# Optimization experiments

Measured on AMD Instinct MI355X. Metric: run time of the kernel, lower is better.

## Reference

```python
import jax, jax.numpy as jnp
import numpy as np

NHEAD = 8
NEG_INF = -1e9
LN_EPS = 1e-5


def setup_inputs() -> dict:
    key = jax.random.key(0)
    ks = jax.random.split(key, 8)
    B, Q, N, C = 2, 256, 16384, 256
    return {
        "queries": jax.random.normal(ks[0], (B, Q, C), jnp.float32),
        "vid_features": jax.random.normal(ks[1], (B, C, N), jnp.float32),
        "vid_mask": jax.random.uniform(ks[2], (B, Q, N), jnp.float32),
        "pos_embed": jax.random.normal(ks[3], (B, C, N), jnp.float32),
        "query_embed": jax.random.normal(ks[4], (B, Q, C), jnp.float32),
        "in_proj_w": jax.random.normal(ks[5], (3 * C, C), jnp.float32) * 0.02,
        "in_proj_b": jnp.zeros((3 * C,), jnp.float32),
        "out_proj_w": jax.random.normal(ks[6], (C, C), jnp.float32) * 0.02,
        "out_proj_b": jnp.zeros((C,), jnp.float32),
        "ln_gamma": jnp.ones((C,), jnp.float32),
        "ln_beta": jnp.zeros((C,), jnp.float32),
    }


def reference(queries, vid_features, vid_mask, pos_embed, query_embed,
              in_proj_w, in_proj_b, out_proj_w, out_proj_b, ln_gamma, ln_beta):
    B, Q, C = queries.shape
    H = NHEAD
    d = C // H

    vf = jnp.transpose(vid_features, (0, 2, 1))   # B N C
    pe = jnp.transpose(pos_embed, (0, 2, 1))      # B N C

    q_in = queries + query_embed                  # with_pos_embed on queries
    k_in = vf + pe                                # with_pos_embed on keys
    v_in = vf

    wq, wk, wv = jnp.split(in_proj_w, 3, axis=0)
    bq, bk, bv = jnp.split(in_proj_b, 3)

    q = (q_in @ wq.T + bq).reshape(B, Q, H, d)
    k = (k_in @ wk.T + bk).reshape(B, -1, H, d)
    v = (v_in @ wv.T + bv).reshape(B, -1, H, d)

    scale = 1.0 / jnp.sqrt(jnp.asarray(d, q.dtype))
    logits = jnp.einsum('bqhd,bnhd->bhqn', q, k) * scale  # B H Q N

    # Hard masking: block keys where mask prob < 0.5; if a query row is
    # fully blocked, fall back to unmasked attention (avoid NaN softmax).
    blocked = vid_mask < 0.5                                 # B Q N
    all_blocked = jnp.all(blocked, axis=-1, keepdims=True)   # B Q 1
    blocked = blocked & jnp.logical_not(all_blocked)
    logits = jnp.where(blocked[:, None, :, :], NEG_INF, logits)

    attn = jax.nn.softmax(logits, axis=-1)
    ctx = jnp.einsum('bhqn,bnhd->bqhd', attn, v).reshape(B, Q, C)
    tgt2 = ctx @ out_proj_w.T + out_proj_b

    # residual + LayerNorm (dropout p=0.0 -> identity)
    x = queries + tgt2
    mu = jnp.mean(x, axis=-1, keepdims=True)
    var = jnp.mean(jnp.square(x - mu), axis=-1, keepdims=True)
    return (x - mu) / jnp.sqrt(var + LN_EPS) * ln_gamma + ln_beta
```

## Files before the change

kernel.cpp:

```cpp
#include <hip/hip_runtime.h>
#include <stdint.h>

#define B_ 2
#define Q_ 256
#define N_ 16384
#define C_ 256
#define H_ 8
#define D_ 32
#define NC_ 32
#define SCALE 0.17677669529663687f

typedef __bf16 bf16x8 __attribute__((ext_vector_type(8)));
typedef float f32x4 __attribute__((ext_vector_type(4)));

__device__ __forceinline__ uint16_t bfbits(float f) {
  union { __bf16 h; uint16_t u; } c;
  c.h = (__bf16)f;
  return c.u;
}
__device__ __forceinline__ uint16_t f2bf(float f) {
  union { float f; uint32_t u; } c; c.f = f;
  uint32_t r = c.u + 0x7FFFu + ((c.u >> 16) & 1u);
  return (uint16_t)(r >> 16);
}
__device__ __forceinline__ uint32_t pk2(float a, float b) {
  return (uint32_t)f2bf(a) | ((uint32_t)f2bf(b) << 16);
}
__device__ __forceinline__ void lgkm0_barrier() {
  __builtin_amdgcn_sched_barrier(0);
  asm volatile("s_waitcnt lgkmcnt(0)" ::: "memory");
  __builtin_amdgcn_sched_barrier(0);
  __builtin_amdgcn_s_barrier();
  __builtin_amdgcn_sched_barrier(0);
}

__global__ __launch_bounds__(256) void prep(const float* __restrict__ inw,
                                            const float* __restrict__ outw,
                                            const float* __restrict__ vm,
                                            uint16_t* __restrict__ wb,
                                            float* __restrict__ woT,
                                            uint32_t* __restrict__ mb) {
  __shared__ __align__(16) char sh[4352];
  const int bid = blockIdx.x;
  const int t = threadIdx.x;
  if (bid < 96) {
    const int i = (bid * 256 + t) * 8;
    const float4 a = *reinterpret_cast<const float4*>(inw + i);
    const float4 b = *reinterpret_cast<const float4*>(inw + i + 4);
    ushort4 lo = {bfbits(a.x), bfbits(a.y), bfbits(a.z), bfbits(a.w)};
    ushort4 hi = {bfbits(b.x), bfbits(b.y), bfbits(b.z), bfbits(b.w)};
    *reinterpret_cast<ushort4*>(wb + i) = lo;
    *reinterpret_cast<ushort4*>(wb + i + 4) = hi;
  } else if (bid < 160) {
    float(*s)[33] = reinterpret_cast<float(*)[33]>(sh);
    const int bb = bid - 96;
    const int bx = bb & 7, by = bb >> 3;
    const int r0 = by * 32, c0 = bx * 32;
    const int tr = t >> 5, tc = t & 31;
#pragma unroll
    for (int k = 0; k < 4; ++k)
      s[tr + 8 * k][tc] = outw[(size_t)(r0 + tr + 8 * k) * 256 + c0 + tc];
    __syncthreads();
#pragma unroll
    for (int k = 0; k < 4; ++k)
      woT[(size_t)(c0 + tr + 8 * k) * 256 + r0 + tc] = s[tc][tr + 8 * k];
  } else {
    uint8_t(*nib)[256] = reinterpret_cast<uint8_t(*)[256]>(sh);
    __shared__ int wcnt[4];
    __shared__ int tot;
    const int bq = bid - 160;
    const float* row = vm + (size_t)bq * N_;
    const int lane = t & 63;
    int cnt = 0;
#pragma unroll
    for (int i = 0; i < 16; ++i) {
      const float4 v = *reinterpret_cast<const float4*>(&row[i * 1024 + 4 * t]);
      const uint32_t nb = (v.x < 0.5f ? 1u : 0u) | (v.y < 0.5f ? 2u : 0u) |
                          (v.z < 0.5f ? 4u : 0u) | (v.w < 0.5f ? 8u : 0u);
      nib[i][t] = (uint8_t)nb;
      cnt += __popc(nb);
    }
    for (int o = 32; o > 0; o >>= 1) cnt += __shfl_down(cnt, o, 64);
    if (lane == 0) wcnt[t >> 6] = cnt;
    __syncthreads();
    if (t == 0) tot = wcnt[0] + wcnt[1] + wcnt[2] + wcnt[3];
    __syncthreads();
    const bool allb = (tot == N_);
    uint32_t* dst = mb + (size_t)bq * 512;
#pragma unroll
    for (int k = 0; k < 2; ++k) {
      const int w = k * 256 + t;
      const int i = w >> 5, tw = w & 31;
      const uint2 u = *reinterpret_cast<const uint2*>(&nib[i][8 * tw]);
      uint32_t y0 = u.x & 0x0F0F0F0Fu; y0 = y0 | (y0 >> 4);
      uint32_t y1 = u.y & 0x0F0F0F0Fu; y1 = y1 | (y1 >> 4);
      const uint32_t word = (y0 & 0xFFu) | (((y0 >> 16) & 0xFFu) << 8) |
                            ((y1 & 0xFFu) << 16) | (((y1 >> 16) & 0xFFu) << 24);
      dst[w] = allb ? 0u : word;
    }
  }
}

__global__ __launch_bounds__(512) void kvqproj(const float* __restrict__ vf,
                                               const float* __restrict__ pe,
                                               const float* __restrict__ queries,
                                               const float* __restrict__ qembed,
                                               const uint16_t* __restrict__ wkv,
                                               const float* __restrict__ bias,
                                               uint16_t* __restrict__ Kb,
                                               uint16_t* __restrict__ Vb,
                                               uint16_t* __restrict__ Qb) {
  __shared__ __align__(16) uint16_t lds[8][64][40];
  const int bid = blockIdx.x;
  const int t = threadIdx.x, wid = t >> 6, lane = t & 63;
  const int g = lane >> 4, c15 = lane & 15;

  if (bid < 1024) {
    const int nb = bid & 511, b = bid >> 9;
    const int n0 = nb * 32;
    const int cin = t >> 1, nh = (t & 1) * 16;
    const int s = cin >> 5, cl = cin & 31;
    const float* Xrow = vf + ((size_t)b * C_ + cin) * N_ + n0 + nh;
    const float* Prow = pe + ((size_t)b * C_ + cin) * N_ + n0 + nh;
    float4 xr4[4], pr4[4];
#pragma unroll
    for (int k = 0; k < 4; ++k) xr4[k] = reinterpret_cast<const float4*>(Xrow)[k];
#pragma unroll
    for (int k = 0; k < 4; ++k) pr4[k] = reinterpret_cast<const float4*>(Prow)[k];
    const float* xf = reinterpret_cast<const float*>(xr4);
    const float* pf = reinterpret_cast<const float*>(pr4);
#pragma unroll
    for (int i = 0; i < 16; ++i) {
      const int n = nh + i;
      const int col = cl ^ (8 * ((n >> 3) & 3));
      lds[s][n][col] = bfbits(xf[i] + pf[i]);
      lds[s][32 + n][col] = bfbits(xf[i]);
    }
    lgkm0_barrier();

    const bool isK = wid < 4;
    const int wc = wid & 3;
    const uint16_t* W = wkv + (isK ? 256 * C_ : 512 * C_);
    f32x4 acc[4][2];
    if (isK) {
#pragma unroll
      for (int cf = 0; cf < 4; ++cf) {
        f32x4 iv;
#pragma unroll
        for (int j = 0; j < 4; ++j) iv[j] = bias[256 + wc * 64 + cf * 16 + 4 * g + j];
        acc[cf][0] = iv;
        acc[cf][1] = iv;
      }
    } else {
#pragma unroll
      for (int cf = 0; cf < 4; ++cf) {
        const float bv = bias[512 + wc * 64 + cf * 16 + c15];
        const f32x4 iv = {bv, bv, bv, bv};
        acc[0][cf] = iv;
        acc[1][cf] = iv;
      }
    }
#pragma unroll
    for (int s8 = 0; s8 < 8; ++s8) {
      bf16x8 Wf[4];
#pragma unroll
      for (int cf = 0; cf < 4; ++cf)
        Wf[cf] = *reinterpret_cast<const bf16x8*>(
            W + (size_t)(wc * 64 + cf * 16 + c15) * C_ + s8 * 32 + g * 8);
      if (isK) {
#pragma unroll
        for (int nf = 0; nf < 2; ++nf) {
          const int r = nf * 16 + c15;
          const bf16x8 Bf = *reinterpret_cast<const bf16x8*>(
              &lds[s8][r][8 * (g ^ ((r >> 3) & 3))]);
#pragma unroll
          for (int cf = 0; cf < 4; ++cf)
            acc[cf][nf] = __builtin_amdgcn_mfma_f32_16x16x32_bf16(Wf[cf], Bf, acc[cf][nf], 0, 0, 0);
        }
      } else {
#pragma unroll
        for (int nf = 0; nf < 2; ++nf) {
          const int r = nf * 16 + c15;
          const bf16x8 Af = *reinterpret_cast<const bf16x8*>(
              &lds[s8][32 + r][8 * (g ^ ((r >> 3) & 3))]);
#pragma unroll
          for (int cf = 0; cf < 4; ++cf)
            acc[nf][cf] = __builtin_amdgcn_mfma_f32_16x16x32_bf16(Af, Wf[cf], acc[nf][cf], 0, 0, 0);
        }
      }
    }
    if (isK) {
      uint16_t* Kp = Kb + (size_t)b * N_ * C_;
#pragma unroll
      for (int cf = 0; cf < 4; ++cf)
#pragma unroll
        for (int nf = 0; nf < 2; ++nf) {
          const f32x4 a = acc[cf][nf];
          uint2 pkv;
          pkv.x = pk2(a[0], a[1]);
          pkv.y = pk2(a[2], a[3]);
          *reinterpret_cast<uint2*>(
              &Kp[(size_t)(n0 + nf * 16 + c15) * C_ + wc * 64 + cf * 16 + 4 * g]) = pkv;
        }
    } else {
      uint16_t* Vp = Vb + (size_t)b * C_ * N_;
#pragma unroll
      for (int nf = 0; nf < 2; ++nf)
#pragma unroll
        for (int cf = 0; cf < 4; ++cf) {
          const f32x4 a = acc[nf][cf];
          uint2 pkv;
          pkv.x = pk2(a[0], a[1]);
          pkv.y = pk2(a[2], a[3]);
          *reinterpret_cast<uint2*>(
              &Vp[(size_t)(wc * 64 + cf * 16 + c15) * N_ + n0 + nf * 16 + 4 * g]) = pkv;
        }
    }
  } else {
    const int qb = bid - 1024;
    const int q0g = qb * 64;
    const int b = q0g >> 8, q0 = q0g & 255;
    const int r = t >> 3, c0 = (t & 7) * 32, s = t & 7;
    const float* Qrow = queries + (size_t)(q0g + r) * C_ + c0;
    const float* Erow = qembed + (size_t)(q0g + r) * C_ + c0;
#pragma unroll
    for (int ph = 0; ph < 2; ++ph) {
      float4 a4[4], e4[4];
#pragma unroll
      for (int k = 0; k < 4; ++k) a4[k] = reinterpret_cast<const float4*>(Qrow + ph * 16)[k];
#pragma unroll
      for (int k = 0; k < 4; ++k) e4[k] = reinterpret_cast<const float4*>(Erow + ph * 16)[k];
      const float* af = reinterpret_cast<const float*>(a4);
      const float* ef = reinterpret_cast<const float*>(e4);
#pragma unroll
      for (int i = 0; i < 16; ++i) {
        const int cl = ph * 16 + i;
        const int col = cl ^ (8 * ((r >> 3) & 3));
        lds[s][r][col] = bfbits(af[i] + ef[i]);
      }
      __builtin_amdgcn_sched_barrier(0);
    }
    lgkm0_barrier();

    const int w = wid;
    f32x4 acc[4][2];
#pragma unroll
    for (int nf = 0; nf < 2; ++nf) {
      const float bv = bias[w * 32 + nf * 16 + c15];
      const f32x4 iv = {bv, bv, bv, bv};
#pragma unroll
      for (int qf = 0; qf < 4; ++qf) acc[qf][nf] = iv;
    }
#pragma unroll
    for (int s8 = 0; s8 < 8; ++s8) {
      bf16x8 Bf[2];
#pragma unroll
      for (int nf = 0; nf < 2; ++nf)
        Bf[nf] = *reinterpret_cast<const bf16x8*>(
            wkv + (size_t)(w * 32 + nf * 16 + c15) * C_ + s8 * 32 + g * 8);
#pragma unroll
      for (int qf = 0; qf < 4; ++qf) {
        const int rr = qf * 16 + c15;
        const bf16x8 Af = *reinterpret_cast<const bf16x8*>(
            &lds[s8][rr][8 * (g ^ ((rr >> 3) & 3))]);
#pragma unroll
        for (int nf = 0; nf < 2; ++nf)
          acc[qf][nf] = __builtin_amdgcn_mfma_f32_16x16x32_bf16(Af, Bf[nf], acc[qf][nf], 0, 0, 0);
      }
    }
#pragma unroll
    for (int qf = 0; qf < 4; ++qf)
#pragma unroll
      for (int nf = 0; nf < 2; ++nf)
#pragma unroll
        for (int j = 0; j < 4; ++j) {
          const int q = q0 + qf * 16 + 4 * g + j;
          const int dk = nf * 16 + c15;
          Qb[((size_t)(b * H_ + w) * Q_ + q) * D_ + dk] = f2bf(acc[qf][nf][j] * SCALE);
        }
  }
}

__global__ __launch_bounds__(512) void attn(const uint16_t* __restrict__ Qb,
                                            const uint16_t* __restrict__ Kb,
                                            const uint16_t* __restrict__ Vb,
                                            const uint32_t* __restrict__ mb,
                                            float* __restrict__ ctx_part,
                                            float* __restrict__ lsum_part) {
  const int bid = blockIdx.x;
  const int nc = bid & 31, h = (bid >> 5) & 7, b = bid >> 8;
  const int t = threadIdx.x, wid = t >> 6, lane = t & 63;
  const int g = lane >> 4, c15 = lane & 15;
  const int qw0 = wid * 32;
  const int nbase = nc * (N_ / NC_);
  constexpr int SS = (N_ / NC_) / 128;

  __shared__ __align__(16) uint16_t kst[2][128][40];
  __shared__ __align__(16) uint16_t vst[2][32][136];
  __shared__ __align__(16) uint16_t plds[8][32][40];

  const uint16_t* Qp = Qb + (size_t)(b * H_ + h) * Q_ * D_;
  bf16x8 qfr[2];
#pragma unroll
  for (int qf = 0; qf < 2; ++qf)
    qfr[qf] = *reinterpret_cast<const bf16x8*>(Qp + (size_t)(qw0 + qf * 16 + c15) * D_ + g * 8);

  f32x4 acc[2][2];
  const f32x4 zero4 = {0.f, 0.f, 0.f, 0.f};
#pragma unroll
  for (int qf = 0; qf < 2; ++qf)
#pragma unroll
    for (int dvf = 0; dvf < 2; ++dvf) acc[qf][dvf] = zero4;
  float lsum[2][4] = {};

  const uint32_t* mrow = mb + (size_t)b * Q_ * (N_ / 32);

  const int krow = t >> 2, kch = t & 3;
  const uint16_t* ksrc = Kb + ((size_t)(b * N_ + nbase + krow)) * C_ + h * D_ + kch * 8;
  const int vrow = t >> 4, vch = t & 15;
  const uint16_t* vsrc = Vb + ((size_t)(b * C_ + h * D_ + vrow)) * N_ + nbase + vch * 8;

  uint4 kreg = *(const uint4*)ksrc;
  uint4 vreg = *(const uint4*)vsrc;

  int cur = 0;
  for (int ss = 0; ss < SS; ++ss) {
    *(uint4*)&kst[cur][krow][kch * 8] = kreg;
    *(uint4*)&vst[cur][vrow][vch * 8] = vreg;
    if (ss < SS - 1) {
      kreg = *(const uint4*)(ksrc + (size_t)(ss + 1) * 128 * C_);
      vreg = *(const uint4*)(vsrc + (ss + 1) * 128);
    }
    lgkm0_barrier();

    const int nstart = nbase + ss * 128;
#pragma unroll
    for (int half = 0; half < 2; ++half) {
      uint32_t mw[2][4][2];
#pragma unroll
      for (int qf = 0; qf < 2; ++qf)
#pragma unroll
        for (int j = 0; j < 4; ++j) {
          const int q = qw0 + qf * 16 + 4 * g + j;
          const uint2 u = *reinterpret_cast<const uint2*>(
              &mrow[(size_t)q * (N_ / 32) + (nstart >> 5) + half * 2]);
          mw[qf][j][0] = u.x;
          mw[qf][j][1] = u.y;
        }
#pragma unroll
      for (int s2 = 0; s2 < 2; ++s2) {
        const int sub = half * 2 + s2;
        const int nl0 = sub * 32;
        bf16x8 kfr[2];
#pragma unroll
        for (int nf = 0; nf < 2; ++nf)
          kfr[nf] = *reinterpret_cast<const bf16x8*>(&kst[cur][nl0 + nf * 16 + c15][g * 8]);
        f32x4 s[2][2];
#pragma unroll
        for (int qf = 0; qf < 2; ++qf)
#pragma unroll
          for (int nf = 0; nf < 2; ++nf)
            s[qf][nf] = __builtin_amdgcn_mfma_f32_16x16x32_bf16(qfr[qf], kfr[nf], zero4, 0, 0, 0);

#pragma unroll
        for (int qf = 0; qf < 2; ++qf) {
#pragma unroll
          for (int j = 0; j < 4; ++j) {
            const uint32_t wmask = mw[qf][j][s2];
#pragma unroll
            for (int nf = 0; nf < 2; ++nf) {
              const int bit = nf * 16 + c15;
              const float p = ((wmask >> bit) & 1u) ? 0.0f : __expf(s[qf][nf][j]);
              lsum[qf][j] += p;
              plds[wid][qf * 16 + 4 * g + j][nf * 16 + c15] = f2bf(p);
            }
          }
        }
        __asm__ volatile("s_waitcnt lgkmcnt(0)" ::: "memory");
#pragma unroll
        for (int qf = 0; qf < 2; ++qf) {
          const bf16x8 pa = *reinterpret_cast<const bf16x8*>(&plds[wid][qf * 16 + c15][g * 8]);
#pragma unroll
          for (int dvf = 0; dvf < 2; ++dvf) {
            const bf16x8 vb =
                *reinterpret_cast<const bf16x8*>(&vst[cur][dvf * 16 + c15][nl0 + g * 8]);
            acc[qf][dvf] = __builtin_amdgcn_mfma_f32_16x16x32_bf16(pa, vb, acc[qf][dvf], 0, 0, 0);
          }
        }
      }
    }
    __builtin_amdgcn_sched_barrier(0);
    cur ^= 1;
  }

#pragma unroll
  for (int qf = 0; qf < 2; ++qf)
#pragma unroll
    for (int j = 0; j < 4; ++j) {
      float v = lsum[qf][j];
      v += __shfl_xor(v, 1, 64);
      v += __shfl_xor(v, 2, 64);
      v += __shfl_xor(v, 4, 64);
      v += __shfl_xor(v, 8, 64);
      lsum[qf][j] = v;
    }

  float* cp = ctx_part + ((size_t)(b * H_ + h) * NC_ + nc) * Q_ * D_;
#pragma unroll
  for (int qf = 0; qf < 2; ++qf)
#pragma unroll
    for (int dvf = 0; dvf < 2; ++dvf)
#pragma unroll
      for (int j = 0; j < 4; ++j) {
        const int q = qw0 + qf * 16 + 4 * g + j;
        cp[(size_t)q * D_ + dvf * 16 + c15] = acc[qf][dvf][j];
      }
  if (c15 == 0) {
    float* lp = lsum_part + ((size_t)(b * H_ + h) * NC_ + nc) * Q_;
#pragma unroll
    for (int qf = 0; qf < 2; ++qf)
#pragma unroll
      for (int j = 0; j < 4; ++j) lp[qw0 + qf * 16 + 4 * g + j] = lsum[qf][j];
  }
}

__global__ __launch_bounds__(256) void epilogue(const float* __restrict__ ctx_part,
                                                const float* __restrict__ lsum_part,
                                                const float* __restrict__ queries,
                                                const float* __restrict__ woT,
                                                const float* __restrict__ bo,
                                                const float* __restrict__ gamma,
                                                const float* __restrict__ beta,
                                                float* __restrict__ out) {
  const int bq = blockIdx.x;
  const int b = bq >> 8, q = bq & 255;
  const int t = threadIdx.x;
  const int h = t >> 5, dv = t & 31;
  float cs = 0.f, ls = 0.f;
  for (int k = 0; k < NC_; ++k) {
    cs += ctx_part[(((size_t)(b * H_ + h) * NC_ + k) * Q_ + q) * D_ + dv];
    ls += lsum_part[((size_t)(b * H_ + h) * NC_ + k) * Q_ + q];
  }
  __shared__ float ctxrow[C_];
  ctxrow[t] = cs / ls;
  __syncthreads();
  float acc = bo[t];
#pragma unroll 8
  for (int j = 0; j < C_; ++j) acc = fmaf(ctxrow[j], woT[(size_t)j * C_ + t], acc);
  const float x = queries[(size_t)bq * C_ + t] + acc;
  float s1 = x, s2 = x * x;
  for (int o = 32; o > 0; o >>= 1) {
    s1 += __shfl_down(s1, o, 64);
    s2 += __shfl_down(s2, o, 64);
  }
  __shared__ float r1[4], r2[4];
  if ((t & 63) == 0) { r1[t >> 6] = s1; r2[t >> 6] = s2; }
  __syncthreads();
  const float mu = (r1[0] + r1[1] + r1[2] + r1[3]) * (1.0f / C_);
  const float e2 = (r2[0] + r2[1] + r2[2] + r2[3]) * (1.0f / C_);
  const float var = e2 - mu * mu;
  out[(size_t)bq * C_ + t] = (x - mu) * rsqrtf(var + 1e-5f) * gamma[t] + beta[t];
}

extern "C" void kernel_launch(void* const* d_in, const int* in_sizes, int n_in,
                              void* d_out, int out_size, void* d_ws, size_t ws_size,
                              hipStream_t stream) {
  const float* queries    = (const float*)d_in[0];
  const float* vidfeat    = (const float*)d_in[1];
  const float* vidmask    = (const float*)d_in[2];
  const float* posembed   = (const float*)d_in[3];
  const float* queryembed = (const float*)d_in[4];
  const float* inw        = (const float*)d_in[5];
  const float* inb        = (const float*)d_in[6];
  const float* outw       = (const float*)d_in[7];
  const float* outb       = (const float*)d_in[8];
  const float* gamma      = (const float*)d_in[9];
  const float* beta       = (const float*)d_in[10];
  float* out = (float*)d_out;

  char* ws = (char*)d_ws;
  size_t off = 0;
  uint16_t* Qb = (uint16_t*)(ws + off); off += (size_t)B_ * H_ * Q_ * D_ * 2;
  uint16_t* Kb = (uint16_t*)(ws + off); off += (size_t)B_ * N_ * C_ * 2;
  uint16_t* Vb = (uint16_t*)(ws + off); off += (size_t)B_ * C_ * N_ * 2;
  uint32_t* mb = (uint32_t*)(ws + off); off += (size_t)B_ * Q_ * (N_ / 32) * 4;
  float* ctxp  = (float*)(ws + off);    off += (size_t)B_ * H_ * NC_ * Q_ * D_ * 4;
  float* lsump = (float*)(ws + off);    off += (size_t)B_ * H_ * NC_ * Q_ * 4;
  uint16_t* wkv = (uint16_t*)(ws + off); off += (size_t)768 * C_ * 2;
  float* woT   = (float*)(ws + off);    off += (size_t)C_ * C_ * 4;

  prep<<<dim3(672), dim3(256), 0, stream>>>(inw, outw, vidmask, wkv, woT, mb);
  kvqproj<<<dim3(1032), dim3(512), 0, stream>>>(vidfeat, posembed, queries, queryembed,
                                                wkv, inb, Kb, Vb, Qb);
  attn<<<dim3(B_ * H_ * NC_), dim3(512), 0, stream>>>(Qb, Kb, Vb, mb, ctxp, lsump);
  epilogue<<<dim3(B_ * Q_), dim3(256), 0, stream>>>(ctxp, lsump, queries, woT, outb, gamma, beta, out);
}
```

Measured before the change: 111.5 us.

## Split K/V projection into bf16 pre-pack pass and register-pipelined GEMMs

The fused K/V/Q projection kernel is split up. A new pass adds the position embedding, converts activations to bf16 and writes them in a channel-group-interleaved layout. Two templated GEMM kernels then read that layout straight into registers, with software-pipelined weight loads, and write K and V in per-head contiguous layouts that the attention kernel now reads. Q projection moves to a scalar fp32 path using a transposed Wq, and the attention partial-sum buffers alias the staging buffers. The aim is to drop the LDS staging and transpose from the projection, at the cost of an extra round trip through global memory and two more launches.

```diff
diff --git a/kernel.cpp b/kernel.cpp
--- a/kernel.cpp
+++ b/kernel.cpp
@@ -39,6 +39,7 @@
                                             const float* __restrict__ vm,
                                             uint16_t* __restrict__ wb,
                                             float* __restrict__ woT,
+                                            float* __restrict__ wqT,
                                             uint32_t* __restrict__ mb) {
   __shared__ __align__(16) char sh[4352];
   const int bid = blockIdx.x;
@@ -47,28 +48,31 @@
     const int i = (bid * 256 + t) * 8;
     const float4 a = *reinterpret_cast<const float4*>(inw + i);
     const float4 b = *reinterpret_cast<const float4*>(inw + i + 4);
-    ushort4 lo = {bfbits(a.x), bfbits(a.y), bfbits(a.z), bfbits(a.w)};
-    ushort4 hi = {bfbits(b.x), bfbits(b.y), bfbits(b.z), bfbits(b.w)};
+    ushort4 lo = {f2bf(a.x), f2bf(a.y), f2bf(a.z), f2bf(a.w)};
+    ushort4 hi = {f2bf(b.x), f2bf(b.y), f2bf(b.z), f2bf(b.w)};
     *reinterpret_cast<ushort4*>(wb + i) = lo;
     *reinterpret_cast<ushort4*>(wb + i + 4) = hi;
-  } else if (bid < 160) {
+  } else if (bid < 224) {
     float(*s)[33] = reinterpret_cast<float(*)[33]>(sh);
-    const int bb = bid - 96;
+    const bool isWo = bid < 160;
+    const int bb = bid - (isWo ? 96 : 160);
+    const float* src = isWo ? outw : inw;
+    float* dst = isWo ? woT : wqT;
     const int bx = bb & 7, by = bb >> 3;
     const int r0 = by * 32, c0 = bx * 32;
     const int tr = t >> 5, tc = t & 31;
 #pragma unroll
     for (int k = 0; k < 4; ++k)
-      s[tr + 8 * k][tc] = outw[(size_t)(r0 + tr + 8 * k) * 256 + c0 + tc];
+      s[tr + 8 * k][tc] = src[(size_t)(r0 + tr + 8 * k) * 256 + c0 + tc];
     __syncthreads();
 #pragma unroll
     for (int k = 0; k < 4; ++k)
-      woT[(size_t)(c0 + tr + 8 * k) * 256 + r0 + tc] = s[tc][tr + 8 * k];
+      dst[(size_t)(c0 + tr + 8 * k) * 256 + r0 + tc] = s[tc][tr + 8 * k];
   } else {
     uint8_t(*nib)[256] = reinterpret_cast<uint8_t(*)[256]>(sh);
     __shared__ int wcnt[4];
     __shared__ int tot;
-    const int bq = bid - 160;
+    const int bq = bid - 224;
     const float* row = vm + (size_t)bq * N_;
     const int lane = t & 63;
     int cnt = 0;
@@ -101,189 +105,192 @@
   }
 }
 
-__global__ __launch_bounds__(512) void kvqproj(const float* __restrict__ vf,
-                                               const float* __restrict__ pe,
-                                               const float* __restrict__ queries,
-                                               const float* __restrict__ qembed,
-                                               const uint16_t* __restrict__ wkv,
-                                               const float* __restrict__ bias,
-                                               uint16_t* __restrict__ Kb,
-                                               uint16_t* __restrict__ Vb,
-                                               uint16_t* __restrict__ Qb) {
-  __shared__ __align__(16) uint16_t lds[8][64][40];
+__global__ __launch_bounds__(256) void fuse(const float* __restrict__ vf,
+                                            const float* __restrict__ pe,
+                                            const float* __restrict__ queries,
+                                            const float* __restrict__ qembed,
+                                            const float* __restrict__ wqT,
+                                            const float* __restrict__ bias,
+                                            uint16_t* __restrict__ XP,
+                                            uint16_t* __restrict__ XV,
+                                            uint16_t* __restrict__ Qb) {
   const int bid = blockIdx.x;
+  const int t = threadIdx.x;
+  if (bid < 1024) {
+    const int b = bid >> 9, cg = (bid >> 4) & 31, ch = bid & 15;
+    const int nq = ch * 1024 + t * 4;
+    const float* vb = vf + ((size_t)(b * 32 + cg) * 8) * N_ + nq;
+    const float* pb = pe + ((size_t)(b * 32 + cg) * 8) * N_ + nq;
+    float4 x[8], p[8];
+#pragma unroll
+    for (int r = 0; r < 8; ++r) x[r] = *reinterpret_cast<const float4*>(vb + (size_t)r * N_);
+#pragma unroll
+    for (int r = 0; r < 8; ++r) p[r] = *reinterpret_cast<const float4*>(pb + (size_t)r * N_);
+    uint16_t* xpo = XP + ((size_t)(b * 32 + cg) * N_ + nq) * 8;
+    uint16_t* xvo = XV + ((size_t)(b * 32 + cg) * N_ + nq) * 8;
+#pragma unroll
+    for (int i = 0; i < 4; ++i) {
+      const float* fx[8];
+      uint4 up, uv;
+      const float x0 = ((const float*)&x[0])[i], x1 = ((const float*)&x[1])[i];
+      const float x2 = ((const float*)&x[2])[i], x3 = ((const float*)&x[3])[i];
+      const float x4 = ((const float*)&x[4])[i], x5 = ((const float*)&x[5])[i];
+      const float x6 = ((const float*)&x[6])[i], x7 = ((const float*)&x[7])[i];
+      const float p0 = ((const float*)&p[0])[i], p1 = ((const float*)&p[1])[i];
+      const float p2 = ((const float*)&p[2])[i], p3 = ((const float*)&p[3])[i];
+      const float p4 = ((const float*)&p[4])[i], p5 = ((const float*)&p[5])[i];
+      const float p6 = ((const float*)&p[6])[i], p7 = ((const float*)&p[7])[i];
+      up.x = pk2(x0 + p0, x1 + p1); up.y = pk2(x2 + p2, x3 + p3);
+      up.z = pk2(x4 + p4, x5 + p5); up.w = pk2(x6 + p6, x7 + p7);
+      uv.x = pk2(x0, x1); uv.y = pk2(x2, x3);
+      uv.z = pk2(x4, x5); uv.w = pk2(x6, x7);
+      *reinterpret_cast<uint4*>(xpo + (size_t)i * 8) = up;
+      *reinterpret_cast<uint4*>(xvo + (size_t)i * 8) = uv;
+      (void)fx;
+    }
+  } else {
+    const int r0 = (bid - 1024) * 4;
+    __shared__ float xq[4][C_];
+#pragma unroll
+    for (int r = 0; r < 4; ++r)
+      xq[r][t] = queries[(size_t)(r0 + r) * C_ + t] + qembed[(size_t)(r0 + r) * C_ + t];
+    __syncthreads();
+    float a0 = bias[t], a1 = a0, a2 = a0, a3 = a0;
+#pragma unroll 4
+    for (int j = 0; j < C_; ++j) {
+      const float wv = wqT[(size_t)j * C_ + t];
+      a0 = fmaf(xq[0][j], wv, a0);
+      a1 = fmaf(xq[1][j], wv, a1);
+      a2 = fmaf(xq[2][j], wv, a2);
+      a3 = fmaf(xq[3][j], wv, a3);
+    }
+    const int h = t >> 5, dk = t & 31;
+    const float r4[4] = {a0, a1, a2, a3};
+#pragma unroll
+    for (int r = 0; r < 4; ++r) {
+      const int bq = r0 + r;
+      const int b = bq >> 8, q = bq & 255;
+      Qb[((size_t)(b * H_ + h) * Q_ + q) * D_ + dk] = f2bf(r4[r] * SCALE);
+    }
+  }
+}
+
+template <int ISK>
+__global__ __launch_bounds__(512, 4) void kvgemm(const uint16_t* __restrict__ Xf,
+                                                 const uint16_t* __restrict__ wkv,
+                                                 const float* __restrict__ bias,
+                                                 uint16_t* __restrict__ outp) {
+  const int bid = blockIdx.x;
+  const int b = bid >> 8, nt = bid & 255;
   const int t = threadIdx.x, wid = t >> 6, lane = t & 63;
   const int g = lane >> 4, c15 = lane & 15;
-
-  if (bid < 1024) {
-    const int nb = bid & 511, b = bid >> 9;
-    const int n0 = nb * 32;
-    const int cin = t >> 1, nh = (t & 1) * 16;
-    const int s = cin >> 5, cl = cin & 31;
-    const float* Xrow = vf + ((size_t)b * C_ + cin) * N_ + n0 + nh;
-    const float* Prow = pe + ((size_t)b * C_ + cin) * N_ + n0 + nh;
-    float4 xr4[4], pr4[4];
-#pragma unroll
-    for (int k = 0; k < 4; ++k) xr4[k] = reinterpret_cast<const float4*>(Xrow)[k];
-#pragma unroll
-    for (int k = 0; k < 4; ++k) pr4[k] = reinterpret_cast<const float4*>(Prow)[k];
-    const float* xf = reinterpret_cast<const float*>(xr4);
-    const float* pf = reinterpret_cast<const float*>(pr4);
-#pragma unroll
-    for (int i = 0; i < 16; ++i) {
-      const int n = nh + i;
-      const int col = cl ^ (8 * ((n >> 3) & 3));
-      lds[s][n][col] = bfbits(xf[i] + pf[i]);
-      lds[s][32 + n][col] = bfbits(xf[i]);
-    }
-    lgkm0_barrier();
-
-    const bool isK = wid < 4;
-    const int wc = wid & 3;
-    const uint16_t* W = wkv + (isK ? 256 * C_ : 512 * C_);
-    f32x4 acc[4][2];
-    if (isK) {
-#pragma unroll
-      for (int cf = 0; cf < 4; ++cf) {
-        f32x4 iv;
-#pragma unroll
-        for (int j = 0; j < 4; ++j) iv[j] = bias[256 + wc * 64 + cf * 16 + 4 * g + j];
-        acc[cf][0] = iv;
-        acc[cf][1] = iv;
+  const int wc = wid & 3;
+  const int n0w = nt * 64 + (wid >> 2) * 32;
+
+  const uint16_t* Wsec = wkv + (ISK ? 256 : 512) * C_ + (size_t)(wc * 64 + c15) * C_;
+  const uint16_t* Xbase = Xf + ((size_t)(b * 32 + g) * N_ + n0w) * 8;
+
+  f32x4 acc[8];
+  if (ISK) {
+#pragma unroll
+    for (int cf = 0; cf < 4; ++cf) {
+      f32x4 iv;
+#pragma unroll
+      for (int j = 0; j < 4; ++j) iv[j] = bias[256 + wc * 64 + cf * 16 + 4 * g + j];
+      acc[cf * 2 + 0] = iv;
+      acc[cf * 2 + 1] = iv;
+    }
+  } else {
+#pragma unroll
+    for (int cf = 0; cf < 4; ++cf) {
+      const float bv = bias[512 + wc * 64 + cf * 16 + c15];
+      const f32x4 iv = {bv, bv, bv, bv};
+      acc[0 * 4 + cf] = iv;
+      acc[1 * 4 + cf] = iv;
+    }
+  }
+
+  bf16x8 Bf[4][2], Wfa[4], Wfb[4];
+
+#define LOADB(s)                                                              \
+  {                                                                           \
+    _Pragma("unroll") for (int nf = 0; nf < 2; ++nf)                          \
+        Bf[(s) & 3][nf] = *reinterpret_cast<const bf16x8*>(                   \
+            Xbase + ((size_t)(s) * 4 * N_ + nf * 16 + c15) * 8);              \
+  }
+#define LOADW(W, s)                                                           \
+  {                                                                           \
+    _Pragma("unroll") for (int cf = 0; cf < 4; ++cf)                          \
+        W[cf] = *reinterpret_cast<const bf16x8*>(                             \
+            Wsec + (size_t)cf * 16 * C_ + (s) * 32 + g * 8);                  \
+  }
+#define COMPUTE(W, s)                                                         \
+  {                                                                           \
+    _Pragma("unroll") for (int nf = 0; nf < 2; ++nf) {                        \
+      if (ISK) {                                                              \
+        _Pragma("unroll") for (int cf = 0; cf < 4; ++cf)                      \
+            acc[cf * 2 + nf] = __builtin_amdgcn_mfma_f32_16x16x32_bf16(       \
+                W[cf], Bf[(s) & 3][nf], acc[cf * 2 + nf], 0, 0, 0);           \
+      } else {                                                                \
+        _Pragma("unroll") for (int cf = 0; cf < 4; ++cf)                      \
+            acc[nf * 4 + cf] = __builtin_amdgcn_mfma_f32_16x16x32_bf16(       \
+                Bf[(s) & 3][nf], W[cf], acc[nf * 4 + cf], 0, 0, 0);           \
+      }                                                                       \
+    }                                                                         \
+  }
+
+  LOADB(0); LOADB(1); LOADB(2); LOADB(3);
+  LOADW(Wfa, 0);
+  LOADB(4); LOADW(Wfb, 1); COMPUTE(Wfa, 0);
+  LOADB(5); LOADW(Wfa, 2); COMPUTE(Wfb, 1);
+  LOADB(6); LOADW(Wfb, 3); COMPUTE(Wfa, 2);
+  LOADB(7); LOADW(Wfa, 4); COMPUTE(Wfb, 3);
+  LOADW(Wfb, 5); COMPUTE(Wfa, 4);
+  LOADW(Wfa, 6); COMPUTE(Wfb, 5);
+  LOADW(Wfb, 7); COMPUTE(Wfa, 6);
+  COMPUTE(Wfb, 7);
+
+#undef LOADB
+#undef LOADW
+#undef COMPUTE
+
+  if (ISK) {
+#pragma unroll
+    for (int cf = 0; cf < 4; ++cf) {
+      const int h = wc * 2 + (cf >> 1);
+      const int dkb = (cf & 1) * 16 + 4 * g;
+#pragma unroll
+      for (int nf = 0; nf < 2; ++nf) {
+        const f32x4 a = acc[cf * 2 + nf];
+        uint2 pkv;
+        pkv.x = pk2(a[0], a[1]);
+        pkv.y = pk2(a[2], a[3]);
+        const int n = n0w + nf * 16 + c15;
+        *reinterpret_cast<uint2*>(
+            &outp[((size_t)(b * H_ + h) * N_ + n) * 32 + dkb]) = pkv;
       }
-    } else {
-#pragma unroll
-      for (int cf = 0; cf < 4; ++cf) {
-        const float bv = bias[512 + wc * 64 + cf * 16 + c15];
-        const f32x4 iv = {bv, bv, bv, bv};
-        acc[0][cf] = iv;
-        acc[1][cf] = iv;
+    }
+  } else {
+#pragma unroll
+    for (int cf = 0; cf < 4; ++cf) {
+      const int cout = wc * 64 + cf * 16 + c15;
+      const int h = cout >> 5, dv = cout & 31;
+#pragma unroll
+      for (int nf = 0; nf < 2; ++nf) {
+        const f32x4 a = acc[nf * 4 + cf];
+        uint2 pkv;
+        pkv.x = pk2(a[0], a[1]);
+        pkv.y = pk2(a[2], a[3]);
+        *reinterpret_cast<uint2*>(
+            &outp[((size_t)(b * H_ + h) * 32 + dv) * N_ + n0w + nf * 16 + 4 * g]) = pkv;
       }
     }
-#pragma unroll
-    for (int s8 = 0; s8 < 8; ++s8) {
-      bf16x8 Wf[4];
-#pragma unroll
-      for (int cf = 0; cf < 4; ++cf)
-        Wf[cf] = *reinterpret_cast<const bf16x8*>(
-            W + (size_t)(wc * 64 + cf * 16 + c15) * C_ + s8 * 32 + g * 8);
-      if (isK) {
-#pragma unroll
-        for (int nf = 0; nf < 2; ++nf) {
-          const int r = nf * 16 + c15;
-          const bf16x8 Bf = *reinterpret_cast<const bf16x8*>(
-              &lds[s8][r][8 * (g ^ ((r >> 3) & 3))]);
-#pragma unroll
-          for (int cf = 0; cf < 4; ++cf)
-            acc[cf][nf] = __builtin_amdgcn_mfma_f32_16x16x32_bf16(Wf[cf], Bf, acc[cf][nf], 0, 0, 0);
-        }
-      } else {
-#pragma unroll
-        for (int nf = 0; nf < 2; ++nf) {
-          const int r = nf * 16 + c15;
-          const bf16x8 Af = *reinterpret_cast<const bf16x8*>(
-              &lds[s8][32 + r][8 * (g ^ ((r >> 3) & 3))]);
-#pragma unroll
-          for (int cf = 0; cf < 4; ++cf)
-            acc[nf][cf] = __builtin_amdgcn_mfma_f32_16x16x32_bf16(Af, Wf[cf], acc[nf][cf], 0, 0, 0);
-        }
-      }
-    }
-    if (isK) {
-      uint16_t* Kp = Kb + (size_t)b * N_ * C_;
-#pragma unroll
-      for (int cf = 0; cf < 4; ++cf)
-#pragma unroll
-        for (int nf = 0; nf < 2; ++nf) {
-          const f32x4 a = acc[cf][nf];
-          uint2 pkv;
-          pkv.x = pk2(a[0], a[1]);
-          pkv.y = pk2(a[2], a[3]);
-          *reinterpret_cast<uint2*>(
-              &Kp[(size_t)(n0 + nf * 16 + c15) * C_ + wc * 64 + cf * 16 + 4 * g]) = pkv;
-        }
-    } else {
-      uint16_t* Vp = Vb + (size_t)b * C_ * N_;
-#pragma unroll
-      for (int nf = 0; nf < 2; ++nf)
-#pragma unroll
-        for (int cf = 0; cf < 4; ++cf) {
-          const f32x4 a = acc[nf][cf];
-          uint2 pkv;
-          pkv.x = pk2(a[0], a[1]);
-          pkv.y = pk2(a[2], a[3]);
-          *reinterpret_cast<uint2*>(
-              &Vp[(size_t)(wc * 64 + cf * 16 + c15) * N_ + n0 + nf * 16 + 4 * g]) = pkv;
-        }
-    }
-  } else {
-    const int qb = bid - 1024;
-    const int q0g = qb * 64;
-    const int b = q0g >> 8, q0 = q0g & 255;
-    const int r = t >> 3, c0 = (t & 7) * 32, s = t & 7;
-    const float* Qrow = queries + (size_t)(q0g + r) * C_ + c0;
-    const float* Erow = qembed + (size_t)(q0g + r) * C_ + c0;
-#pragma unroll
-    for (int ph = 0; ph < 2; ++ph) {
-      float4 a4[4], e4[4];
-#pragma unroll
-      for (int k = 0; k < 4; ++k) a4[k] = reinterpret_cast<const float4*>(Qrow + ph * 16)[k];
-#pragma unroll
-      for (int k = 0; k < 4; ++k) e4[k] = reinterpret_cast<const float4*>(Erow + ph * 16)[k];
-      const float* af = reinterpret_cast<const float*>(a4);
-      const float* ef = reinterpret_cast<const float*>(e4);
-#pragma unroll
-      for (int i = 0; i < 16; ++i) {
-        const int cl = ph * 16 + i;
-        const int col = cl ^ (8 * ((r >> 3) & 3));
-        lds[s][r][col] = bfbits(af[i] + ef[i]);
-      }
-      __builtin_amdgcn_sched_barrier(0);
-    }
-    lgkm0_barrier();
-
-    const int w = wid;
-    f32x4 acc[4][2];
-#pragma unroll
-    for (int nf = 0; nf < 2; ++nf) {
-      const float bv = bias[w * 32 + nf * 16 + c15];
-      const f32x4 iv = {bv, bv, bv, bv};
-#pragma unroll
-      for (int qf = 0; qf < 4; ++qf) acc[qf][nf] = iv;
-    }
-#pragma unroll
-    for (int s8 = 0; s8 < 8; ++s8) {
-      bf16x8 Bf[2];
-#pragma unroll
-      for (int nf = 0; nf < 2; ++nf)
-        Bf[nf] = *reinterpret_cast<const bf16x8*>(
-            wkv + (size_t)(w * 32 + nf * 16 + c15) * C_ + s8 * 32 + g * 8);
-#pragma unroll
-      for (int qf = 0; qf < 4; ++qf) {
-        const int rr = qf * 16 + c15;
-        const bf16x8 Af = *reinterpret_cast<const bf16x8*>(
-            &lds[s8][rr][8 * (g ^ ((rr >> 3) & 3))]);
-#pragma unroll
-        for (int nf = 0; nf < 2; ++nf)
-          acc[qf][nf] = __builtin_amdgcn_mfma_f32_16x16x32_bf16(Af, Bf[nf], acc[qf][nf], 0, 0, 0);
-      }
-    }
-#pragma unroll
-    for (int qf = 0; qf < 4; ++qf)
-#pragma unroll
-      for (int nf = 0; nf < 2; ++nf)
-#pragma unroll
-        for (int j = 0; j < 4; ++j) {
-          const int q = q0 + qf * 16 + 4 * g + j;
-          const int dk = nf * 16 + c15;
-          Qb[((size_t)(b * H_ + w) * Q_ + q) * D_ + dk] = f2bf(acc[qf][nf][j] * SCALE);
-        }
   }
 }
 
 __global__ __launch_bounds__(512) void attn(const uint16_t* __restrict__ Qb,
-                                            const uint16_t* __restrict__ Kb,
-                                            const uint16_t* __restrict__ Vb,
+                                            const uint16_t* __restrict__ Kh,
+                                            const uint16_t* __restrict__ Vh,
                                             const uint32_t* __restrict__ mb,
                                             float* __restrict__ ctx_part,
                                             float* __restrict__ lsum_part) {
@@ -316,9 +323,9 @@
   const uint32_t* mrow = mb + (size_t)b * Q_ * (N_ / 32);
 
   const int krow = t >> 2, kch = t & 3;
-  const uint16_t* ksrc = Kb + ((size_t)(b * N_ + nbase + krow)) * C_ + h * D_ + kch * 8;
+  const uint16_t* ksrc = Kh + ((size_t)(b * H_ + h) * N_ + nbase + krow) * 32 + kch * 8;
   const int vrow = t >> 4, vch = t & 15;
-  const uint16_t* vsrc = Vb + ((size_t)(b * C_ + h * D_ + vrow)) * N_ + nbase + vch * 8;
+  const uint16_t* vsrc = Vh + ((size_t)(b * H_ + h) * 32 + vrow) * N_ + nbase + vch * 8;
 
   uint4 kreg = *(const uint4*)ksrc;
   uint4 vreg = *(const uint4*)vsrc;
@@ -328,7 +335,7 @@
     *(uint4*)&kst[cur][krow][kch * 8] = kreg;
     *(uint4*)&vst[cur][vrow][vch * 8] = vreg;
     if (ss < SS - 1) {
-      kreg = *(const uint4*)(ksrc + (size_t)(ss + 1) * 128 * C_);
+      kreg = *(const uint4*)(ksrc + (size_t)(ss + 1) * 128 * 32);
       vreg = *(const uint4*)(vsrc + (ss + 1) * 128);
     }
     lgkm0_barrier();
@@ -480,18 +487,24 @@
 
   char* ws = (char*)d_ws;
   size_t off = 0;
-  uint16_t* Qb = (uint16_t*)(ws + off); off += (size_t)B_ * H_ * Q_ * D_ * 2;
-  uint16_t* Kb = (uint16_t*)(ws + off); off += (size_t)B_ * N_ * C_ * 2;
-  uint16_t* Vb = (uint16_t*)(ws + off); off += (size_t)B_ * C_ * N_ * 2;
-  uint32_t* mb = (uint32_t*)(ws + off); off += (size_t)B_ * Q_ * (N_ / 32) * 4;
-  float* ctxp  = (float*)(ws + off);    off += (size_t)B_ * H_ * NC_ * Q_ * D_ * 4;
-  float* lsump = (float*)(ws + off);    off += (size_t)B_ * H_ * NC_ * Q_ * 4;
+  uint16_t* Qb  = (uint16_t*)(ws + off); off += (size_t)B_ * H_ * Q_ * D_ * 2;
+  uint16_t* Kh  = (uint16_t*)(ws + off); off += (size_t)B_ * H_ * N_ * D_ * 2;
+  uint16_t* Vh  = (uint16_t*)(ws + off); off += (size_t)B_ * H_ * D_ * N_ * 2;
+  uint32_t* mb  = (uint32_t*)(ws + off); off += (size_t)B_ * Q_ * (N_ / 32) * 4;
   uint16_t* wkv = (uint16_t*)(ws + off); off += (size_t)768 * C_ * 2;
-  float* woT   = (float*)(ws + off);    off += (size_t)C_ * C_ * 4;
-
-  prep<<<dim3(672), dim3(256), 0, stream>>>(inw, outw, vidmask, wkv, woT, mb);
-  kvqproj<<<dim3(1032), dim3(512), 0, stream>>>(vidfeat, posembed, queries, queryembed,
-                                                wkv, inb, Kb, Vb, Qb);
-  attn<<<dim3(B_ * H_ * NC_), dim3(512), 0, stream>>>(Qb, Kb, Vb, mb, ctxp, lsump);
-  epilogue<<<dim3(B_ * Q_), dim3(256), 0, stream>>>(ctxp, lsump, queries, woT, outb, gamma, beta, out);
-}
+  float* woT    = (float*)(ws + off);    off += (size_t)C_ * C_ * 4;
+  float* wqT    = (float*)(ws + off);    off += (size_t)C_ * C_ * 4;
+  uint16_t* XP  = (uint16_t*)(ws + off); off += (size_t)B_ * C_ * N_ * 2;
+  uint16_t* XV  = (uint16_t*)(ws + off); off += (size_t)B_ * C_ * N_ * 2;
+  float* ctxp  = (float*)XP;
+  float* lsump = (float*)XV;
+
+  prep<<<dim3(736), dim3(256), 0, stream>>>(inw, outw, vidmask, wkv, woT, wqT, mb);
+  fuse<<<dim3(1152), dim3(256), 0, stream>>>(vidfeat, posembed, queries, queryembed,
+                                             wqT, inb, XP, XV, Qb);
+  kvgemm<1><<<dim3(512), dim3(512), 0, stream>>>(XP, wkv, inb, Kh);
+  kvgemm<0><<<dim3(512), dim3(512), 0, stream>>>(XV, wkv, inb, Vh);
+  attn<<<dim3(B_ * H_ * NC_), dim3(512), 0, stream>>>(Qb, Kh, Vh, mb, ctxp, lsump);
+  epilogue<<<dim3(B_ * Q_), dim3(256), 0, stream>>>(ctxp, lsump, queries, woT, outb,
+                                                    gamma, beta, out);
+}
```

Result: slower. 133.1 us (+19.4%).
